# Optimization experiments

Measured on AMD Instinct MI355X. Metric: run time of the kernel, lower is better.

## Reference

```python
import jax, jax.numpy as jnp
import numpy as np

BN = 128  # weight block rows
BK = 128  # quantization block along K
FP8_MAX = 448.0  # float8_e4m3fn max finite value
F8 = jnp.float8_e4m3fn


def _quant_dequant_act(x):
    # Dynamic per-token, per-128-block FP8 quantization (scale = amax/448), then dequant.
    M, K = x.shape
    xb = x.reshape(M, K // BK, BK)
    amax = jnp.max(jnp.abs(xb), axis=-1, keepdims=True)
    scale = jnp.maximum(amax, 1e-12) / FP8_MAX
    q = jnp.clip(xb / scale, -FP8_MAX, FP8_MAX).astype(F8)
    return (q.astype(jnp.float32) * scale).reshape(M, K)


def _dequant_weight(w, s):
    # w: (N, K) fp8, s: (N//BN, K//BK) f32 block scales
    N, K = w.shape
    sf = jnp.repeat(jnp.repeat(s, BN, axis=0), BK, axis=1)[:N, :K]
    return w.astype(jnp.float32) * sf


def _fp8_linear(x, w, s):
    # y = dequant(quant(x)) @ dequant(w)^T  -- matches w8a8_fp8_matmul semantics
    return _quant_dequant_act(x) @ _dequant_weight(w, s).T


def _quantize_weight(key, shape):
    E, N, K = shape
    w = jax.random.normal(key, shape, jnp.float32) * 0.02
    wb = w.reshape(E, N // BN, BN, K // BK, BK)
    amax = jnp.max(jnp.abs(wb), axis=(2, 4), keepdims=True)
    scale = jnp.maximum(amax, 1e-12) / FP8_MAX
    q = jnp.clip(wb / scale, -FP8_MAX, FP8_MAX).astype(F8).reshape(E, N, K)
    return q, scale.reshape(E, N // BN, K // BK)


def setup_inputs() -> dict:
    key = jax.random.key(0)
    k1, k2, k3, k4, k5 = jax.random.split(key, 5)
    T, H, I, E, TOPK = 2048, 2048, 1408, 8, 2
    hidden_states = jax.random.normal(k1, (T, H), jnp.float32)
    top_k_index = jax.random.randint(k2, (T, TOPK), 0, E).astype(jnp.int64)
    w = jax.random.uniform(k3, (T, TOPK), jnp.float32)
    top_k_weights = w / jnp.sum(w, axis=-1, keepdims=True)
    gate_up_proj, gate_up_proj_scale_inv = _quantize_weight(k4, (E, 2 * I, H))
    down_proj, down_proj_scale_inv = _quantize_weight(k5, (E, H, I))
    return {
        "hidden_states": hidden_states,
        "top_k_index": top_k_index,
        "top_k_weights": top_k_weights,
        "gate_up_proj": gate_up_proj,
        "gate_up_proj_scale_inv": gate_up_proj_scale_inv,
        "down_proj": down_proj,
        "down_proj_scale_inv": down_proj_scale_inv,
    }


def reference(hidden_states, top_k_index, top_k_weights, gate_up_proj,
              gate_up_proj_scale_inv, down_proj, down_proj_scale_inv):
    E = gate_up_proj.shape[0]
    I = down_proj.shape[-1]
    # Activation quantization is per-token: identical for every expert, compute once.
    x_dq = _quant_dequant_act(hidden_states)  # (T, H)
    out = jnp.zeros_like(hidden_states, dtype=jnp.float32)
    for e in range(E):  # fixed small expert loop (structural, not data dim)
        gu = x_dq @ _dequant_weight(gate_up_proj[e], gate_up_proj_scale_inv[e]).T  # (T, 2I)
        gate, up = gu[:, :I], gu[:, I:]
        h = jax.nn.silu(gate) * up
        d = _fp8_linear(h, down_proj[e], down_proj_scale_inv[e])  # (T, H)
        # routing weight for this expert per token (sums duplicates like index_add_)
        rw = jnp.sum(jnp.where(top_k_index == e, top_k_weights, 0.0), axis=-1)  # (T,)
        out = out + rw[:, None] * d
    return out.astype(hidden_states.dtype)
```

## Files before the change

kernel.cpp:

```cpp
#include <hip/hip_runtime.h>
#include <cstdint>
#include <cstddef>

using f32x4 = __attribute__((ext_vector_type(4))) float;

#define TDIM 2048
#define HDIM 2048
#define IDIM 1408
#define NEXP 8
#define NKB1 16
#define NKB2 11
#define MAXM 4096
#define N8GUP 5767168
#define N8DWN 2883584

__device__ __forceinline__ void gll16(const void* g, void* l) {
  __builtin_amdgcn_global_load_lds(
      (__attribute__((address_space(1))) void*)(uintptr_t)g,
      (__attribute__((address_space(3))) void*)(uint32_t)(uintptr_t)l,
      16, 0, 0);
}

__device__ __forceinline__ f32x4 mfma_fp8(long a, long b, f32x4 c) {
  return __builtin_amdgcn_mfma_f32_16x16x32_fp8_fp8(a, b, c, 0, 0, 0);
}

__device__ __forceinline__ uint32_t f8_1(float q) {
  q = fminf(fmaxf(q, -448.f), 448.f);
  return (uint32_t)__builtin_amdgcn_cvt_pk_fp8_f32(q, q, 0, false) & 0xffu;
}

__device__ __forceinline__ float bf16_to_f32(uint32_t bits16) {
  union { uint32_t u; float f; } c;
  c.u = bits16 << 16;
  return c.f;
}

__global__ void sniff_kernel(const uint16_t* __restrict__ a,
                             const uint16_t* __restrict__ b,
                             int* __restrict__ modes, int* __restrict__ cnt) {
  if (threadIdx.x < 8) cnt[threadIdx.x] = 0;
  if (threadIdx.x == 0) {
    unsigned acc = 0;
    for (int i = 0; i < 128; ++i) acc |= a[2 * i];
    modes[0] = (acc == 0) ? 1 : 0;
    acc = 0;
    for (int i = 0; i < 128; ++i) acc |= b[2 * i];
    modes[1] = (acc == 0) ? 1 : 0;
  }
}

__global__ void repack_kernel(const void* __restrict__ gup, const void* __restrict__ dwn,
                              uint8_t* __restrict__ gq, uint8_t* __restrict__ dq,
                              const int* __restrict__ modes) {
  int i = blockIdx.x * 256 + threadIdx.x;
  const void* in;
  uint8_t* out;
  int midx;
  if (i < N8GUP) { in = gup; out = gq; midx = 0; }
  else {
    i -= N8GUP;
    if (i >= N8DWN) return;
    in = dwn; out = dq; midx = 1;
  }
  const int m = modes[midx];
  float f[8];
  if (m == 1) {
    const float4* p = (const float4*)in;
    float4 a = p[2 * i], b = p[2 * i + 1];
    f[0] = a.x; f[1] = a.y; f[2] = a.z; f[3] = a.w;
    f[4] = b.x; f[5] = b.y; f[6] = b.z; f[7] = b.w;
  } else {
    uint4 v = ((const uint4*)in)[i];
#pragma unroll
    for (int j = 0; j < 4; ++j) {
      uint32_t w = (&v.x)[j];
      f[2 * j]     = bf16_to_f32(w & 0xffffu);
      f[2 * j + 1] = bf16_to_f32(w >> 16);
    }
  }
  uint32_t lo = 0, hi = 0;
#pragma unroll
  for (int j = 0; j < 8; ++j) {
    uint32_t b8 = f8_1(f[j]);
    if (j < 4) lo |= b8 << (8 * j);
    else       hi |= b8 << (8 * (j - 4));
  }
  ((uint2*)out)[i] = make_uint2(lo, hi);
}

__global__ void quantx_kernel(const float* __restrict__ x,
                              uint8_t* __restrict__ xq, float* __restrict__ xs) {
  const int gid = blockIdx.x * 8 + (threadIdx.x >> 5);
  const int l = threadIdx.x & 31;
  const int r = gid >> 4, kb = gid & 15;
  const float* base = x + (size_t)r * HDIM + kb * 128 + l * 4;
  const f32x4 v = *(const f32x4*)base;
  float a = fmaxf(fmaxf(fabsf(v[0]), fabsf(v[1])), fmaxf(fabsf(v[2]), fabsf(v[3])));
#pragma unroll
  for (int d = 1; d < 32; d <<= 1) a = fmaxf(a, __shfl_xor(a, d));
  const float s = fmaxf(a, 1e-12f) / 448.f;
  uint32_t pk = 0;
#pragma unroll
  for (int j = 0; j < 4; ++j) pk |= f8_1(v[j] / s) << (8 * j);
  *(uint32_t*)(xq + (size_t)r * HDIM + kb * 128 + l * 4) = pk;
  if (l == 0) xs[r * 16 + kb] = s;
}

__global__ void route_kernel(const void* __restrict__ idxraw,
                             int* __restrict__ list, int* __restrict__ cnt) {
  const long long* p = (const long long*)idxraw;
  unsigned hi = 0;
#pragma unroll
  for (int j = 0; j < 16; ++j) hi |= (unsigned)((unsigned long long)p[j] >> 32);
  const int i = blockIdx.x * 256 + threadIdx.x;
  int e;
  if (hi == 0) {
    e = (int)p[i];
  } else {
    long long v = p[i >> 1];
    e = (int)((i & 1) ? (v >> 32) : (v & 0xffffffffLL));
  }
  e &= 7;
  const int pos = atomicAdd(&cnt[e], 1);
  list[e * MAXM + pos] = i;
}

__global__ __launch_bounds__(256) void gemm1_kernel(
    const uint8_t* __restrict__ xq, const float* __restrict__ xs,
    const uint8_t* __restrict__ w, const float* __restrict__ wscl,
    const int* __restrict__ list, const int* __restrict__ cnt,
    uint8_t* __restrict__ hq, float* __restrict__ hs) {
  const int e = blockIdx.z, mt = blockIdx.y, nb = blockIdx.x;
  const int M = cnt[e];
  if (mt * 64 >= M) return;
  __shared__ __align__(16) uint8_t As[8192];
  __shared__ __align__(16) uint8_t Bg[2 * 16384];
  __shared__ __align__(16) uint8_t Bu[2 * 16384];
  __shared__ int slots[64];
  __shared__ __align__(16) float sxsAll[16][64];
  __shared__ __align__(16) float amx[128];
  const int tid = threadIdx.x, lane = tid & 63, wid = tid >> 6;
  const int wr = wid >> 1, wc = wid & 1;
  if (tid < 64) {
    int m = mt * 64 + tid;
    slots[tid] = list[e * MAXM + (m < M ? m : 0)];
  }
  __syncthreads();
  {
    const int r = tid >> 2, q = tid & 3;
    const int tok = slots[r] >> 1;
    f32x4 v = *(const f32x4*)(xs + (size_t)tok * 16 + q * 4);
    sxsAll[q * 4 + 0][r] = v[0];
    sxsAll[q * 4 + 1][r] = v[1];
    sxsAll[q * 4 + 2][r] = v[2];
    sxsAll[q * 4 + 3][r] = v[3];
  }
  const int s = tid >> 3;
  const int cj0 = ((tid & 7) ^ (s & 7)) << 4;
  const long tokA0 = slots[s] >> 1;
  const long tokA1 = slots[s + 32] >> 1;
  const uint8_t* pA0 = xq + tokA0 * HDIM + cj0;
  const uint8_t* pA1 = xq + tokA1 * HDIM + cj0;
  const size_t wb = (size_t)e * (2 * IDIM) * HDIM;
  const uint8_t* pG = w + wb + (size_t)(nb * 128 + s) * HDIM + cj0;
  const uint8_t* pU = w + wb + (size_t)(IDIM + nb * 128 + s) * HDIM + cj0;
  const float* wsg = wscl + (size_t)e * 352 + nb * 16;
  const float* wsu = wsg + 176;
  f32x4 accg[2][4] = {};
  f32x4 accu[2][4] = {};
  const int kbyte = (lane >> 4) << 3;
#define STAGEB(d, kk) { const int ko_ = (kk) << 7; \
    _Pragma("unroll") \
    for (int k = 0; k < 4; ++k) { \
      gll16(pG + (size_t)(k * 32) * HDIM + ko_, Bg + (d) * 16384 + k * 4096 + tid * 16); \
      gll16(pU + (size_t)(k * 32) * HDIM + ko_, Bu + (d) * 16384 + k * 4096 + tid * 16); \
    } }
  f32x4 rA0 = *(const f32x4*)(pA0);
  f32x4 rA1 = *(const f32x4*)(pA1);
  STAGEB(0, 0)
  __syncthreads();
  int cur = 0;
  for (int kb = 0; kb < NKB1; ++kb) {
    *(f32x4*)(As + tid * 16) = rA0;
    *(f32x4*)(As + 4096 + tid * 16) = rA1;
    if (kb + 1 < NKB1) {
      STAGEB(cur ^ 1, kb + 1)
      const int ko = (kb + 1) << 7;
      rA0 = *(const f32x4*)(pA0 + ko);
      rA1 = *(const f32x4*)(pA1 + ko);
    }
    asm volatile("s_waitcnt lgkmcnt(0)" ::: "memory");
    __builtin_amdgcn_s_barrier();
    const float swg = wsg[kb];
    const float swu = wsu[kb];
    const uint8_t* Bgb = Bg + cur * 16384;
    const uint8_t* Bub = Bu + cur * 16384;
    long af[2][4], bgf[4][4], buf_[4][4];
#pragma unroll
    for (int mi = 0; mi < 2; ++mi) {
      const int r = wr * 32 + mi * 16 + (lane & 15);
      const int xr = (r & 7) << 4;
      const uint8_t* bp = As + r * 128;
#pragma unroll
      for (int kc = 0; kc < 4; ++kc)
        af[mi][kc] = *(const long*)(bp + (((kc << 5) + kbyte) ^ xr));
    }
#pragma unroll
    for (int ni = 0; ni < 4; ++ni) {
      const int r = wc * 64 + ni * 16 + (lane & 15);
      const int xr = (r & 7) << 4;
      const uint8_t* bpg = Bgb + r * 128;
      const uint8_t* bpu = Bub + r * 128;
#pragma unroll
      for (int kc = 0; kc < 4; ++kc) {
        bgf[ni][kc] = *(const long*)(bpg + (((kc << 5) + kbyte) ^ xr));
        buf_[ni][kc] = *(const long*)(bpu + (((kc << 5) + kbyte) ^ xr));
      }
    }
    f32x4 sxg[2], sxu[2];
#pragma unroll
    for (int mi = 0; mi < 2; ++mi) {
      f32x4 sx = *(const f32x4*)(&sxsAll[kb][wr * 32 + mi * 16 + ((lane >> 4) << 2)]);
      sxg[mi] = sx * swg;
      sxu[mi] = sx * swu;
    }
    asm volatile("s_waitcnt lgkmcnt(0)" ::: "memory");
    __builtin_amdgcn_sched_barrier(0);
#pragma unroll
    for (int mi = 0; mi < 2; ++mi)
#pragma unroll
      for (int ni = 0; ni < 4; ++ni) {
        f32x4 pg = {0.f, 0.f, 0.f, 0.f};
        f32x4 pu = {0.f, 0.f, 0.f, 0.f};
#pragma unroll
        for (int kc = 0; kc < 4; ++kc) {
          pg = mfma_fp8(af[mi][kc], bgf[ni][kc], pg);
          pu = mfma_fp8(af[mi][kc], buf_[ni][kc], pu);
        }
#pragma unroll
        for (int j = 0; j < 4; ++j) {
          accg[mi][ni][j] += pg[j] * sxg[mi][j];
          accu[mi][ni][j] += pu[j] * sxu[mi][j];
        }
      }
    asm volatile("s_waitcnt vmcnt(0)" ::: "memory");
    __builtin_amdgcn_s_barrier();
    cur ^= 1;
  }
#undef STAGEB
  f32x4 hv[2][4];
  f32x4 rmax[2];
#pragma unroll
  for (int mi = 0; mi < 2; ++mi) {
#pragma unroll
    for (int ni = 0; ni < 4; ++ni)
#pragma unroll
      for (int j = 0; j < 4; ++j) {
        float g = accg[mi][ni][j];
        float u = accu[mi][ni][j];
        float h = (g / (1.f + expf(-g))) * u;
        hv[mi][ni][j] = h;
        float ah = fabsf(h);
        rmax[mi][j] = (ni == 0) ? ah : fmaxf(rmax[mi][j], ah);
      }
#pragma unroll
    for (int d = 1; d < 16; d <<= 1)
#pragma unroll
      for (int j = 0; j < 4; ++j)
        rmax[mi][j] = fmaxf(rmax[mi][j], __shfl_xor(rmax[mi][j], d));
  }
  __syncthreads();
  if ((lane & 15) == 0) {
#pragma unroll
    for (int mi = 0; mi < 2; ++mi)
#pragma unroll
      for (int j = 0; j < 4; ++j) {
        int row = wr * 32 + mi * 16 + ((lane >> 4) << 2) + j;
        amx[row * 2 + wc] = rmax[mi][j];
      }
  }
  __syncthreads();
  const int Mrem = M - mt * 64;
#pragma unroll
  for (int mi = 0; mi < 2; ++mi)
#pragma unroll
    for (int j = 0; j < 4; ++j) {
      const int row = wr * 32 + mi * 16 + ((lane >> 4) << 2) + j;
      float am = fmaxf(amx[row * 2], amx[row * 2 + 1]);
      float sq = fmaxf(am, 1e-12f) / 448.f;
      if (row < Mrem) {
        const int slot = slots[row];
        uint8_t* hp = hq + (size_t)slot * IDIM + nb * 128 + wc * 64 + (lane & 15);
#pragma unroll
        for (int ni = 0; ni < 4; ++ni)
          hp[ni * 16] = (uint8_t)f8_1(hv[mi][ni][j] / sq);
        if (wc == 0 && (lane & 15) == 0) hs[slot * 16 + nb] = sq;
      }
    }
}

__global__ __launch_bounds__(256) void gemm2_kernel(
    const uint8_t* __restrict__ hq, const float* __restrict__ hs,
    const uint8_t* __restrict__ w, const float* __restrict__ wscl,
    const int* __restrict__ list, const int* __restrict__ cnt,
    const float* __restrict__ tkw, float* __restrict__ tmp) {
  const int e = blockIdx.z, mt = blockIdx.y, nt = blockIdx.x;
  const int M = cnt[e];
  if (mt * 64 >= M) return;
  __shared__ __align__(16) uint8_t As[8192];
  __shared__ __align__(16) uint8_t Bs[2 * 16384];
  __shared__ int slots[64];
  __shared__ float rwl[64];
  __shared__ __align__(16) float sxsAll[16][64];
  const int tid = threadIdx.x, lane = tid & 63, wid = tid >> 6;
  const int wr = wid >> 1, wc = wid & 1;
  if (tid < 64) {
    int m = mt * 64 + tid;
    int slot = list[e * MAXM + (m < M ? m : 0)];
    slots[tid] = slot;
    rwl[tid] = (m < M) ? tkw[slot] : 0.f;
  }
  __syncthreads();
  {
    const int r = tid >> 2, q = tid & 3;
    const float* ps = hs + (size_t)slots[r] * 16;
    f32x4 v = *(const f32x4*)(ps + q * 4);
    sxsAll[q * 4 + 0][r] = v[0];
    sxsAll[q * 4 + 1][r] = v[1];
    sxsAll[q * 4 + 2][r] = v[2];
    sxsAll[q * 4 + 3][r] = v[3];
  }
  const int s = tid >> 3;
  const int cj0 = ((tid & 7) ^ (s & 7)) << 4;
  const long sA0 = slots[s];
  const long sA1 = slots[s + 32];
  const uint8_t* pA0 = hq + sA0 * IDIM + cj0;
  const uint8_t* pA1 = hq + sA1 * IDIM + cj0;
  const uint8_t* pB = w + (size_t)e * HDIM * IDIM + (size_t)(nt * 128 + s) * IDIM + cj0;
  const float* wsd = wscl + (size_t)e * 176 + nt * 11;
  f32x4 acc[2][4] = {};
  const int kbyte = (lane >> 4) << 3;
#define STAGEB2(d, kk) { const int ko_ = (kk) << 7; \
    _Pragma("unroll") \
    for (int k = 0; k < 4; ++k) \
      gll16(pB + (size_t)(k * 32) * IDIM + ko_, Bs + (d) * 16384 + k * 4096 + tid * 16); }
  f32x4 rA0 = *(const f32x4*)(pA0);
  f32x4 rA1 = *(const f32x4*)(pA1);
  STAGEB2(0, 0)
  __syncthreads();
  int cur = 0;
  for (int kb = 0; kb < NKB2; ++kb) {
    *(f32x4*)(As + tid * 16) = rA0;
    *(f32x4*)(As + 4096 + tid * 16) = rA1;
    if (kb + 1 < NKB2) {
      STAGEB2(cur ^ 1, kb + 1)
      const int ko = (kb + 1) << 7;
      rA0 = *(const f32x4*)(pA0 + ko);
      rA1 = *(const f32x4*)(pA1 + ko);
    }
    asm volatile("s_waitcnt lgkmcnt(0)" ::: "memory");
    __builtin_amdgcn_s_barrier();
    const float swd = wsd[kb];
    const uint8_t* Bb = Bs + cur * 16384;
    long af[2][4], bf[4][4];
#pragma unroll
    for (int mi = 0; mi < 2; ++mi) {
      const int r = wr * 32 + mi * 16 + (lane & 15);
      const int xr = (r & 7) << 4;
      const uint8_t* bp = As + r * 128;
#pragma unroll
      for (int kc = 0; kc < 4; ++kc)
        af[mi][kc] = *(const long*)(bp + (((kc << 5) + kbyte) ^ xr));
    }
#pragma unroll
    for (int ni = 0; ni < 4; ++ni) {
      const int r = wc * 64 + ni * 16 + (lane & 15);
      const int xr = (r & 7) << 4;
      const uint8_t* bp = Bb + r * 128;
#pragma unroll
      for (int kc = 0; kc < 4; ++kc)
        bf[ni][kc] = *(const long*)(bp + (((kc << 5) + kbyte) ^ xr));
    }
    f32x4 sxd[2];
#pragma unroll
    for (int mi = 0; mi < 2; ++mi) {
      f32x4 sx = *(const f32x4*)(&sxsAll[kb][wr * 32 + mi * 16 + ((lane >> 4) << 2)]);
      sxd[mi] = sx * swd;
    }
    asm volatile("s_waitcnt lgkmcnt(0)" ::: "memory");
    __builtin_amdgcn_sched_barrier(0);
#pragma unroll
    for (int mi = 0; mi < 2; ++mi)
#pragma unroll
      for (int ni = 0; ni < 4; ++ni) {
        f32x4 p = {0.f, 0.f, 0.f, 0.f};
#pragma unroll
        for (int kc = 0; kc < 4; ++kc) p = mfma_fp8(af[mi][kc], bf[ni][kc], p);
#pragma unroll
        for (int j = 0; j < 4; ++j) acc[mi][ni][j] += p[j] * sxd[mi][j];
      }
    asm volatile("s_waitcnt vmcnt(0)" ::: "memory");
    __builtin_amdgcn_s_barrier();
    cur ^= 1;
  }
#undef STAGEB2
  const int Mrem = M - mt * 64;
#pragma unroll
  for (int mi = 0; mi < 2; ++mi)
#pragma unroll
    for (int j = 0; j < 4; ++j) {
      const int row = wr * 32 + mi * 16 + ((lane >> 4) << 2) + j;
      if (row < Mrem) {
        const int slot = slots[row];
        const float rw = rwl[row];
        float* op = tmp + (size_t)slot * HDIM + nt * 128 + wc * 64 + (lane & 15);
#pragma unroll
        for (int ni = 0; ni < 4; ++ni) op[ni * 16] = rw * acc[mi][ni][j];
      }
    }
}

__global__ void reduce_kernel(const float* __restrict__ tmp, float* __restrict__ out) {
  const int i = blockIdx.x * 256 + threadIdx.x;
  const int t = i >> 9, c4 = i & 511;
  const f32x4 a = ((const f32x4*)tmp)[(size_t)(2 * t) * 512 + c4];
  const f32x4 c = ((const f32x4*)tmp)[(size_t)(2 * t) * 512 + 512 + c4];
  ((f32x4*)out)[i] = a + c;
}

extern "C" void kernel_launch(void* const* d_in, const int* in_sizes, int n_in,
                              void* d_out, int out_size, void* d_ws, size_t ws_size,
                              hipStream_t stream) {
  const float* hidden = (const float*)d_in[0];
  const void* topk_idx = d_in[1];
  const float* topk_w = (const float*)d_in[2];
  const void* gup_raw = d_in[3];
  const float* gup_s = (const float*)d_in[4];
  const void* dwn_raw = d_in[5];
  const float* dwn_s = (const float*)d_in[6];
  float* out = (float*)d_out;
  uint8_t* ws = (uint8_t*)d_ws;
  uint8_t* xq = ws;
  float* xs = (float*)(ws + 4194304);
  uint8_t* hq = ws + 4325376;
  float* hs = (float*)(ws + 10092544);
  int* list = (int*)(ws + 10354688);
  int* cnt = (int*)(ws + 10485760);
  int* modes = (int*)(ws + 10485824);
  uint8_t* gq = ws + 10485888;
  float* tmp = (float*)gq;
  uint8_t* dq = ws + 56623232;
  (void)in_sizes; (void)n_in; (void)ws_size; (void)out_size;

  sniff_kernel<<<1, 64, 0, stream>>>((const uint16_t*)gup_raw, (const uint16_t*)dwn_raw, modes, cnt);
  repack_kernel<<<(N8GUP + N8DWN + 255) / 256, 256, 0, stream>>>(gup_raw, dwn_raw, gq, dq, modes);
  quantx_kernel<<<4096, 256, 0, stream>>>(hidden, xq, xs);
  route_kernel<<<16, 256, 0, stream>>>(topk_idx, list, cnt);
  gemm1_kernel<<<dim3(11, 64, 8), 256, 0, stream>>>(xq, xs, gq, gup_s, list, cnt, hq, hs);
  gemm2_kernel<<<dim3(16, 64, 8), 256, 0, stream>>>(hq, hs, dq, dwn_s, list, cnt, topk_w, tmp);
  reduce_kernel<<<4096, 256, 0, stream>>>(tmp, out);
}
```

Before: 216.8 us.

## Load A fragments directly from global into registers, skip LDS staging

Both grouped GEMM kernels now load the activation (A) MFMA fragments straight from global memory into registers with a two-set double buffer, removing the LDS A tile, its writes, and the LDS fragment reads. The wait is relaxed to a partial vmcnt so that only the previous stage's loads must complete before the barrier. Per-block weight scales are also preloaded into shared memory once instead of read from global each iteration. The direct A loads are 8-byte scattered per lane, not 16-byte coalesced, and the vmcnt counts must exactly match the number of outstanding loads per stage.

```diff
diff --git a/kernel.cpp b/kernel.cpp
--- a/kernel.cpp
+++ b/kernel.cpp
@@ -134,17 +134,22 @@
   const int e = blockIdx.z, mt = blockIdx.y, nb = blockIdx.x;
   const int M = cnt[e];
   if (mt * 64 >= M) return;
-  __shared__ __align__(16) uint8_t As[8192];
   __shared__ __align__(16) uint8_t Bg[2 * 16384];
   __shared__ __align__(16) uint8_t Bu[2 * 16384];
   __shared__ int slots[64];
   __shared__ __align__(16) float sxsAll[16][64];
   __shared__ __align__(16) float amx[128];
+  __shared__ float wsl[32];
   const int tid = threadIdx.x, lane = tid & 63, wid = tid >> 6;
   const int wr = wid >> 1, wc = wid & 1;
+  const float* wsg = wscl + (size_t)e * 352 + nb * 16;
   if (tid < 64) {
     int m = mt * 64 + tid;
     slots[tid] = list[e * MAXM + (m < M ? m : 0)];
+  }
+  if (tid >= 224) {
+    int t = tid - 224;
+    wsl[t] = (t < 16) ? wsg[t] : wsg[176 + (t - 16)];
   }
   __syncthreads();
   {
@@ -158,54 +163,50 @@
   }
   const int s = tid >> 3;
   const int cj0 = ((tid & 7) ^ (s & 7)) << 4;
-  const long tokA0 = slots[s] >> 1;
-  const long tokA1 = slots[s + 32] >> 1;
-  const uint8_t* pA0 = xq + tokA0 * HDIM + cj0;
-  const uint8_t* pA1 = xq + tokA1 * HDIM + cj0;
   const size_t wb = (size_t)e * (2 * IDIM) * HDIM;
   const uint8_t* pG = w + wb + (size_t)(nb * 128 + s) * HDIM + cj0;
   const uint8_t* pU = w + wb + (size_t)(IDIM + nb * 128 + s) * HDIM + cj0;
-  const float* wsg = wscl + (size_t)e * 352 + nb * 16;
-  const float* wsu = wsg + 176;
+  const int kbyte = (lane >> 4) << 3;
+  const int ar = wr * 32 + (lane & 15);
+  const long tA0 = slots[ar] >> 1;
+  const long tA1 = slots[ar + 16] >> 1;
+  const uint8_t* pAm0 = xq + tA0 * HDIM + kbyte;
+  const uint8_t* pAm1 = xq + tA1 * HDIM + kbyte;
   f32x4 accg[2][4] = {};
   f32x4 accu[2][4] = {};
-  const int kbyte = (lane >> 4) << 3;
+  int cur = 0;
 #define STAGEB(d, kk) { const int ko_ = (kk) << 7; \
     _Pragma("unroll") \
     for (int k = 0; k < 4; ++k) { \
       gll16(pG + (size_t)(k * 32) * HDIM + ko_, Bg + (d) * 16384 + k * 4096 + tid * 16); \
       gll16(pU + (size_t)(k * 32) * HDIM + ko_, Bu + (d) * 16384 + k * 4096 + tid * 16); \
     } }
-  f32x4 rA0 = *(const f32x4*)(pA0);
-  f32x4 rA1 = *(const f32x4*)(pA1);
+#define LOADAF(d0, d1, kk) { const int ko_ = (kk) << 7; \
+    _Pragma("unroll") \
+    for (int kc = 0; kc < 4; ++kc) { \
+      d0[kc] = *(const long*)(pAm0 + ko_ + kc * 32); \
+      d1[kc] = *(const long*)(pAm1 + ko_ + kc * 32); \
+    } }
+  long afA0[4], afA1[4], afB0[4], afB1[4];
+  LOADAF(afA0, afA1, 0)
   STAGEB(0, 0)
   __syncthreads();
-  int cur = 0;
-  for (int kb = 0; kb < NKB1; ++kb) {
-    *(f32x4*)(As + tid * 16) = rA0;
-    *(f32x4*)(As + 4096 + tid * 16) = rA1;
-    if (kb + 1 < NKB1) {
+  auto body = [&](int kb, long (&aR0)[4], long (&aR1)[4],
+                  long (&aW0)[4], long (&aW1)[4]) {
+    const bool notlast = (kb + 1 < NKB1);
+    if (notlast) {
+      LOADAF(aW0, aW1, kb + 1)
       STAGEB(cur ^ 1, kb + 1)
-      const int ko = (kb + 1) << 7;
-      rA0 = *(const f32x4*)(pA0 + ko);
-      rA1 = *(const f32x4*)(pA1 + ko);
-    }
-    asm volatile("s_waitcnt lgkmcnt(0)" ::: "memory");
+      asm volatile("s_waitcnt vmcnt(16)" ::: "memory");
+    } else {
+      asm volatile("s_waitcnt vmcnt(0)" ::: "memory");
+    }
     __builtin_amdgcn_s_barrier();
-    const float swg = wsg[kb];
-    const float swu = wsu[kb];
+    const float swg = wsl[kb];
+    const float swu = wsl[16 + kb];
     const uint8_t* Bgb = Bg + cur * 16384;
     const uint8_t* Bub = Bu + cur * 16384;
-    long af[2][4], bgf[4][4], buf_[4][4];
-#pragma unroll
-    for (int mi = 0; mi < 2; ++mi) {
-      const int r = wr * 32 + mi * 16 + (lane & 15);
-      const int xr = (r & 7) << 4;
-      const uint8_t* bp = As + r * 128;
-#pragma unroll
-      for (int kc = 0; kc < 4; ++kc)
-        af[mi][kc] = *(const long*)(bp + (((kc << 5) + kbyte) ^ xr));
-    }
+    long bgf[4][4], buf_[4][4];
 #pragma unroll
     for (int ni = 0; ni < 4; ++ni) {
       const int r = wc * 64 + ni * 16 + (lane & 15);
@@ -228,15 +229,16 @@
     asm volatile("s_waitcnt lgkmcnt(0)" ::: "memory");
     __builtin_amdgcn_sched_barrier(0);
 #pragma unroll
-    for (int mi = 0; mi < 2; ++mi)
+    for (int mi = 0; mi < 2; ++mi) {
+      long* aR = (mi == 0) ? aR0 : aR1;
 #pragma unroll
       for (int ni = 0; ni < 4; ++ni) {
         f32x4 pg = {0.f, 0.f, 0.f, 0.f};
         f32x4 pu = {0.f, 0.f, 0.f, 0.f};
 #pragma unroll
         for (int kc = 0; kc < 4; ++kc) {
-          pg = mfma_fp8(af[mi][kc], bgf[ni][kc], pg);
-          pu = mfma_fp8(af[mi][kc], buf_[ni][kc], pu);
+          pg = mfma_fp8(aR[kc], bgf[ni][kc], pg);
+          pu = mfma_fp8(aR[kc], buf_[ni][kc], pu);
         }
 #pragma unroll
         for (int j = 0; j < 4; ++j) {
@@ -244,11 +246,16 @@
           accu[mi][ni][j] += pu[j] * sxu[mi][j];
         }
       }
-    asm volatile("s_waitcnt vmcnt(0)" ::: "memory");
+    }
     __builtin_amdgcn_s_barrier();
     cur ^= 1;
+  };
+  for (int kb = 0; kb < NKB1; kb += 2) {
+    body(kb, afA0, afA1, afB0, afB1);
+    body(kb + 1, afB0, afB1, afA0, afA1);
   }
 #undef STAGEB
+#undef LOADAF
   f32x4 hv[2][4];
   f32x4 rmax[2];
 #pragma unroll
@@ -308,18 +315,23 @@
   const int e = blockIdx.z, mt = blockIdx.y, nt = blockIdx.x;
   const int M = cnt[e];
   if (mt * 64 >= M) return;
-  __shared__ __align__(16) uint8_t As[8192];
   __shared__ __align__(16) uint8_t Bs[2 * 16384];
   __shared__ int slots[64];
   __shared__ float rwl[64];
   __shared__ __align__(16) float sxsAll[16][64];
+  __shared__ float wsl2[16];
   const int tid = threadIdx.x, lane = tid & 63, wid = tid >> 6;
   const int wr = wid >> 1, wc = wid & 1;
+  const float* wsd = wscl + (size_t)e * 176 + nt * 11;
   if (tid < 64) {
     int m = mt * 64 + tid;
     int slot = list[e * MAXM + (m < M ? m : 0)];
     slots[tid] = slot;
     rwl[tid] = (m < M) ? tkw[slot] : 0.f;
+  }
+  if (tid >= 240) {
+    int t = tid - 240;
+    if (t < NKB2) wsl2[t] = wsd[t];
   }
   __syncthreads();
   {
@@ -333,46 +345,43 @@
   }
   const int s = tid >> 3;
   const int cj0 = ((tid & 7) ^ (s & 7)) << 4;
-  const long sA0 = slots[s];
-  const long sA1 = slots[s + 32];
-  const uint8_t* pA0 = hq + sA0 * IDIM + cj0;
-  const uint8_t* pA1 = hq + sA1 * IDIM + cj0;
   const uint8_t* pB = w + (size_t)e * HDIM * IDIM + (size_t)(nt * 128 + s) * IDIM + cj0;
-  const float* wsd = wscl + (size_t)e * 176 + nt * 11;
+  const int kbyte = (lane >> 4) << 3;
+  const int ar = wr * 32 + (lane & 15);
+  const long sl0 = slots[ar];
+  const long sl1 = slots[ar + 16];
+  const uint8_t* pAm0 = hq + sl0 * IDIM + kbyte;
+  const uint8_t* pAm1 = hq + sl1 * IDIM + kbyte;
   f32x4 acc[2][4] = {};
-  const int kbyte = (lane >> 4) << 3;
+  int cur = 0;
 #define STAGEB2(d, kk) { const int ko_ = (kk) << 7; \
     _Pragma("unroll") \
     for (int k = 0; k < 4; ++k) \
       gll16(pB + (size_t)(k * 32) * IDIM + ko_, Bs + (d) * 16384 + k * 4096 + tid * 16); }
-  f32x4 rA0 = *(const f32x4*)(pA0);
-  f32x4 rA1 = *(const f32x4*)(pA1);
+#define LOADAF2(d0, d1, kk) { const int ko_ = (kk) << 7; \
+    _Pragma("unroll") \
+    for (int kc = 0; kc < 4; ++kc) { \
+      d0[kc] = *(const long*)(pAm0 + ko_ + kc * 32); \
+      d1[kc] = *(const long*)(pAm1 + ko_ + kc * 32); \
+    } }
+  long afA0[4], afA1[4], afB0[4], afB1[4];
+  LOADAF2(afA0, afA1, 0)
   STAGEB2(0, 0)
   __syncthreads();
-  int cur = 0;
-  for (int kb = 0; kb < NKB2; ++kb) {
-    *(f32x4*)(As + tid * 16) = rA0;
-    *(f32x4*)(As + 4096 + tid * 16) = rA1;
-    if (kb + 1 < NKB2) {
+  auto body = [&](int kb, long (&aR0)[4], long (&aR1)[4],
+                  long (&aW0)[4], long (&aW1)[4]) {
+    const bool notlast = (kb + 1 < NKB2);
+    if (notlast) {
+      LOADAF2(aW0, aW1, kb + 1)
       STAGEB2(cur ^ 1, kb + 1)
-      const int ko = (kb + 1) << 7;
-      rA0 = *(const f32x4*)(pA0 + ko);
-      rA1 = *(const f32x4*)(pA1 + ko);
-    }
-    asm volatile("s_waitcnt lgkmcnt(0)" ::: "memory");
+      asm volatile("s_waitcnt vmcnt(12)" ::: "memory");
+    } else {
+      asm volatile("s_waitcnt vmcnt(0)" ::: "memory");
+    }
     __builtin_amdgcn_s_barrier();
-    const float swd = wsd[kb];
+    const float swd = wsl2[kb];
     const uint8_t* Bb = Bs + cur * 16384;
-    long af[2][4], bf[4][4];
-#pragma unroll
-    for (int mi = 0; mi < 2; ++mi) {
-      const int r = wr * 32 + mi * 16 + (lane & 15);
-      const int xr = (r & 7) << 4;
-      const uint8_t* bp = As + r * 128;
-#pragma unroll
-      for (int kc = 0; kc < 4; ++kc)
-        af[mi][kc] = *(const long*)(bp + (((kc << 5) + kbyte) ^ xr));
-    }
+    long bf[4][4];
 #pragma unroll
     for (int ni = 0; ni < 4; ++ni) {
       const int r = wc * 64 + ni * 16 + (lane & 15);
@@ -391,20 +400,27 @@
     asm volatile("s_waitcnt lgkmcnt(0)" ::: "memory");
     __builtin_amdgcn_sched_barrier(0);
 #pragma unroll
-    for (int mi = 0; mi < 2; ++mi)
+    for (int mi = 0; mi < 2; ++mi) {
+      long* aR = (mi == 0) ? aR0 : aR1;
 #pragma unroll
       for (int ni = 0; ni < 4; ++ni) {
         f32x4 p = {0.f, 0.f, 0.f, 0.f};
 #pragma unroll
-        for (int kc = 0; kc < 4; ++kc) p = mfma_fp8(af[mi][kc], bf[ni][kc], p);
+        for (int kc = 0; kc < 4; ++kc) p = mfma_fp8(aR[kc], bf[ni][kc], p);
 #pragma unroll
         for (int j = 0; j < 4; ++j) acc[mi][ni][j] += p[j] * sxd[mi][j];
       }
-    asm volatile("s_waitcnt vmcnt(0)" ::: "memory");
+    }
     __builtin_amdgcn_s_barrier();
     cur ^= 1;
-  }
+  };
+  for (int kb = 0; kb + 2 <= NKB2; kb += 2) {
+    body(kb, afA0, afA1, afB0, afB1);
+    body(kb + 1, afB0, afB1, afA0, afA1);
+  }
+  body(NKB2 - 1, afA0, afA1, afB0, afB1);
 #undef STAGEB2
+#undef LOADAF2
   const int Mrem = M - mt * 64;
 #pragma unroll
   for (int mi = 0; mi < 2; ++mi)
```

Result: slower. 306.1 us (+41.2%).
